# Kernel tuning notes

Measured on AMD Instinct MI355X. Metric: run time of the kernel, lower is better.

## Reference

```python
import jax, jax.numpy as jnp
import numpy as np

N_NODES = 50000


def sage_conv(x, edge_index, W_l, b_l, W_r):
    # PyG SAGEConv (mean aggr): out_i = lin_l(mean_{j->i} x_j) + lin_r(x_i)
    src, dst = edge_index[0], edge_index[1]
    msgs = x[src]                                        # [E, C] gather
    summed = jax.ops.segment_sum(msgs, dst, num_segments=N_NODES)  # [N, C]
    deg = jax.ops.segment_sum(jnp.ones((edge_index.shape[1],), x.dtype), dst,
                              num_segments=N_NODES)
    mean = summed / jnp.maximum(deg, 1.0)[:, None]
    return mean @ W_l + b_l + x @ W_r


def setup_inputs() -> dict:
    key = jax.random.key(0)
    ks = jax.random.split(key, 12)
    E, EL, C, X = 800000, 1000000, 128, 384
    return {
        "x": jax.random.normal(ks[0], (N_NODES, X), jnp.float32),
        "edge_index": jax.random.randint(ks[1], (2, E), 0, N_NODES),
        "edge_label_index": jax.random.randint(ks[2], (2, EL), 0, N_NODES),
        "W_lin": jax.random.normal(ks[3], (X, C), jnp.float32) * 0.05,
        "b_lin": jax.random.normal(ks[4], (C,), jnp.float32) * 0.05,
        "W1_l": jax.random.normal(ks[5], (C, C), jnp.float32) * 0.08,
        "b1": jax.random.normal(ks[6], (C,), jnp.float32) * 0.05,
        "W1_r": jax.random.normal(ks[7], (C, C), jnp.float32) * 0.08,
        "W2_l": jax.random.normal(ks[8], (C, C), jnp.float32) * 0.08,
        "b2": jax.random.normal(ks[9], (C,), jnp.float32) * 0.05,
        "W2_r": jax.random.normal(ks[10], (C, C), jnp.float32) * 0.08,
    }


def reference(x, edge_index, edge_label_index, W_lin, b_lin,
              W1_l, b1, W1_r, W2_l, b2, W2_r):
    h = x @ W_lin + b_lin                                # label_lin
    h = jax.nn.relu(sage_conv(h, edge_index, W1_l, b1, W1_r))
    h = sage_conv(h, edge_index, W2_l, b2, W2_r)
    # Classifier: dot product of head/tail node features per label edge
    head = h[edge_label_index[0]]
    tail = h[edge_label_index[1]]
    return (head * tail).sum(axis=-1)                    # [EL]
```

## Files before the change

### kernel.cpp

```cpp
#include <hip/hip_runtime.h>

#define NODES 50000
#define CH 128
#define ELLW 64

using frag_ab = __attribute__((ext_vector_type(8))) short;
using frag_cd = __attribute__((ext_vector_type(4))) float;

__device__ __forceinline__ float bf2f(ushort u) {
    union { unsigned u; float f; } v; v.u = ((unsigned)u) << 16; return v.f;
}
__device__ __forceinline__ ushort f2bf(float f) {
    union { float f; unsigned u; } v; v.f = f;
    unsigned r = v.u + 0x7fff + ((v.u >> 16) & 1);
    return (ushort)(r >> 16);
}

__global__ void prep_weights(const float* __restrict__ Wlin,
                             const float* __restrict__ W1l, const float* __restrict__ W1r,
                             const float* __restrict__ W2l, const float* __restrict__ W2r,
                             ushort* __restrict__ o0, ushort* __restrict__ o1,
                             ushort* __restrict__ o2, ushort* __restrict__ o3,
                             ushort* __restrict__ o4, int* __restrict__ deg) {
    int b = blockIdx.x;
    if (b >= 448) {
        int i = (b - 448) * 256 + threadIdx.y * 128 + threadIdx.x;
        if (i < NODES) deg[i] = 0;
        return;
    }
    const float* W; ushort* O; int K; int kb;
    if (b < 192) { W = Wlin; O = o0; K = 384; kb = b; }
    else {
        int j = (b - 192) >> 6; kb = (b - 192) & 63; K = 128;
        W = (j == 0) ? W1l : (j == 1) ? W1r : (j == 2) ? W2l : W2r;
        O = (j == 0) ? o1  : (j == 1) ? o2  : (j == 2) ? o3  : o4;
    }
    int k = kb * 2 + threadIdx.y;
    int n = threadIdx.x;
    if (k < K) O[(size_t)n * K + k] = f2bf(W[(size_t)k * 128 + n]);
}

__global__ void fill_ell(const int* __restrict__ ei, int E,
                         int* __restrict__ deg, int* __restrict__ ell) {
    int e = blockIdx.x * blockDim.x + threadIdx.x;
    if (e < E) {
        int d = ei[E + e];
        int pos = atomicAdd(&deg[d], 1);
        if (pos < ELLW) ell[(size_t)d * ELLW + pos] = ei[e];
    }
}

__device__ __forceinline__ void acc8(float* acc, uint4 v) {
    acc[0] += bf2f((ushort)(v.x & 0xffff)); acc[1] += bf2f((ushort)(v.x >> 16));
    acc[2] += bf2f((ushort)(v.y & 0xffff)); acc[3] += bf2f((ushort)(v.y >> 16));
    acc[4] += bf2f((ushort)(v.z & 0xffff)); acc[5] += bf2f((ushort)(v.z >> 16));
    acc[6] += bf2f((ushort)(v.w & 0xffff)); acc[7] += bf2f((ushort)(v.w >> 16));
}

__global__ __launch_bounds__(256) void aggregate_ell(
    const ushort* __restrict__ h, const int* __restrict__ ell,
    const int* __restrict__ deg, ushort* __restrict__ mean, int N) {
    int node = blockIdx.x * 4 + (threadIdx.x >> 6);
    if (node >= N) return;
    int lane = threadIdx.x & 63;
    int g = lane >> 4;
    int q = lane & 15;
    const int* row = ell + (size_t)node * ELLW;
    int d = deg[node];
    int dc = d < ELLW ? d : ELLW;

    float acc[8];
#pragma unroll
    for (int k = 0; k < 8; ++k) acc[k] = 0.f;

    int n = 0;
    for (; n + 16 <= dc; n += 16) {
        int i0 = row[n + g];
        int i1 = row[n + 4 + g];
        int i2 = row[n + 8 + g];
        int i3 = row[n + 12 + g];
        uint4 v0 = *(const uint4*)(h + (size_t)i0 * CH + q * 8);
        uint4 v1 = *(const uint4*)(h + (size_t)i1 * CH + q * 8);
        uint4 v2 = *(const uint4*)(h + (size_t)i2 * CH + q * 8);
        uint4 v3 = *(const uint4*)(h + (size_t)i3 * CH + q * 8);
        acc8(acc, v0); acc8(acc, v1); acc8(acc, v2); acc8(acc, v3);
    }
    for (; n + 8 <= dc; n += 8) {
        int i0 = row[n + g];
        int i1 = row[n + 4 + g];
        uint4 v0 = *(const uint4*)(h + (size_t)i0 * CH + q * 8);
        uint4 v1 = *(const uint4*)(h + (size_t)i1 * CH + q * 8);
        acc8(acc, v0); acc8(acc, v1);
    }
    for (; n < dc; n += 4) {
        int j = n + g;
        if (j < dc) {
            int i0 = row[j];
            uint4 v0 = *(const uint4*)(h + (size_t)i0 * CH + q * 8);
            acc8(acc, v0);
        }
    }
#pragma unroll
    for (int k = 0; k < 8; ++k) {
        acc[k] += __shfl_xor(acc[k], 16, 64);
        acc[k] += __shfl_xor(acc[k], 32, 64);
    }
    if (g == 0) {
        float inv = 1.f / fmaxf((float)d, 1.f);
        uint4 o;
        o.x = ((uint)f2bf(acc[1] * inv) << 16) | (uint)f2bf(acc[0] * inv);
        o.y = ((uint)f2bf(acc[3] * inv) << 16) | (uint)f2bf(acc[2] * inv);
        o.z = ((uint)f2bf(acc[5] * inv) << 16) | (uint)f2bf(acc[4] * inv);
        o.w = ((uint)f2bf(acc[7] * inv) << 16) | (uint)f2bf(acc[6] * inv);
        *(uint4*)(mean + (size_t)node * CH + q * 8) = o;
    }
}

__global__ __launch_bounds__(256) void gemm_lin(
    const float* __restrict__ A, const ushort* __restrict__ Wt,
    const float* __restrict__ bias, ushort* __restrict__ out, int N)
{
    __shared__ ushort As[128 * 32];
    __shared__ ushort Bs[128 * 32];
    const int tid = threadIdx.x;
    const int lane = tid & 63;
    const int wave = tid >> 6;
    const int wr = wave >> 1, wc = wave & 1;
    const int row0 = blockIdx.x * 128;
    const int l15 = lane & 15, quad = lane >> 4;

    frag_cd acc[4][4];
#pragma unroll
    for (int i = 0; i < 4; ++i)
#pragma unroll
        for (int j = 0; j < 4; ++j) acc[i][j] = (frag_cd){0.f, 0.f, 0.f, 0.f};

#pragma unroll 1
    for (int k0 = 0; k0 < 384; k0 += 32) {
        __syncthreads();
#pragma unroll
        for (int i = 0; i < 4; ++i) {
            int e = i * 256 + tid;
            int r = e >> 3, q = e & 7;
            int gr = row0 + r; if (gr > N - 1) gr = N - 1;
            float4 v = *(const float4*)(A + (size_t)gr * 384 + k0 + q * 4);
            ushort4 o; o.x = f2bf(v.x); o.y = f2bf(v.y); o.z = f2bf(v.z); o.w = f2bf(v.w);
            *(ushort4*)(As + r * 32 + q * 4) = o;
        }
#pragma unroll
        for (int i = 0; i < 2; ++i) {
            int e = i * 256 + tid;
            uint4 v = *(const uint4*)(Wt + (size_t)(e >> 2) * 384 + k0 + (e & 3) * 8);
            *(uint4*)(Bs + e * 8) = v;
        }
        __syncthreads();

        frag_ab a[4], b[4];
#pragma unroll
        for (int i = 0; i < 4; ++i)
            a[i] = *(const frag_ab*)(As + (wr * 64 + i * 16 + l15) * 32 + quad * 8);
#pragma unroll
        for (int j = 0; j < 4; ++j)
            b[j] = *(const frag_ab*)(Bs + (wc * 64 + j * 16 + l15) * 32 + quad * 8);
#pragma unroll
        for (int i = 0; i < 4; ++i)
#pragma unroll
            for (int j = 0; j < 4; ++j)
                acc[i][j] = __builtin_amdgcn_mfma_f32_16x16x32_bf16(a[i], b[j], acc[i][j], 0, 0, 0);
    }

#pragma unroll
    for (int i = 0; i < 4; ++i)
#pragma unroll
        for (int r = 0; r < 4; ++r) {
            int row = row0 + wr * 64 + i * 16 + quad * 4 + r;
            if (row < N)
#pragma unroll
                for (int j = 0; j < 4; ++j) {
                    int col = wc * 64 + j * 16 + l15;
                    out[(size_t)row * 128 + col] = f2bf(acc[i][j][r] + bias[col]);
                }
        }
}

template <bool RELU>
__global__ __launch_bounds__(256) void mfma_gemm(
    const ushort* __restrict__ A1, const ushort* __restrict__ Wt1,
    const ushort* __restrict__ A2, const ushort* __restrict__ Wt2,
    const float* __restrict__ bias, ushort* __restrict__ out, int N)
{
    __shared__ ushort As[128 * 32];
    __shared__ ushort Bs[128 * 32];
    const int tid = threadIdx.x;
    const int lane = tid & 63;
    const int wave = tid >> 6;
    const int wr = wave >> 1, wc = wave & 1;
    const int row0 = blockIdx.x * 128;
    const int l15 = lane & 15, quad = lane >> 4;

    frag_cd acc[4][4];
#pragma unroll
    for (int i = 0; i < 4; ++i)
#pragma unroll
        for (int j = 0; j < 4; ++j) acc[i][j] = (frag_cd){0.f, 0.f, 0.f, 0.f};

#pragma unroll 1
    for (int part = 0; part < 2; ++part) {
        const ushort* A  = part ? A2 : A1;
        const ushort* Wt = part ? Wt2 : Wt1;

#pragma unroll 1
        for (int k0 = 0; k0 < 128; k0 += 32) {
            __syncthreads();
#pragma unroll
            for (int i = 0; i < 2; ++i) {
                int e = i * 256 + tid;
                int r = e >> 2, kq = e & 3;
                int gr = row0 + r; if (gr > N - 1) gr = N - 1;
                uint4 v = *(const uint4*)(A + (size_t)gr * 128 + k0 + kq * 8);
                *(uint4*)(As + e * 8) = v;
            }
#pragma unroll
            for (int i = 0; i < 2; ++i) {
                int e = i * 256 + tid;
                uint4 v = *(const uint4*)(Wt + (size_t)(e >> 2) * 128 + k0 + (e & 3) * 8);
                *(uint4*)(Bs + e * 8) = v;
            }
            __syncthreads();

            frag_ab a[4], b[4];
#pragma unroll
            for (int i = 0; i < 4; ++i)
                a[i] = *(const frag_ab*)(As + (wr * 64 + i * 16 + l15) * 32 + quad * 8);
#pragma unroll
            for (int j = 0; j < 4; ++j)
                b[j] = *(const frag_ab*)(Bs + (wc * 64 + j * 16 + l15) * 32 + quad * 8);
#pragma unroll
            for (int i = 0; i < 4; ++i)
#pragma unroll
                for (int j = 0; j < 4; ++j)
                    acc[i][j] = __builtin_amdgcn_mfma_f32_16x16x32_bf16(a[i], b[j], acc[i][j], 0, 0, 0);
        }
    }

#pragma unroll
    for (int i = 0; i < 4; ++i)
#pragma unroll
        for (int r = 0; r < 4; ++r) {
            int row = row0 + wr * 64 + i * 16 + quad * 4 + r;
            if (row < N)
#pragma unroll
                for (int j = 0; j < 4; ++j) {
                    int col = wc * 64 + j * 16 + l15;
                    float v = acc[i][j][r] + bias[col];
                    if (RELU) v = fmaxf(v, 0.f);
                    out[(size_t)row * 128 + col] = f2bf(v);
                }
        }
}

__device__ __forceinline__ float dot8(uint4 va, uint4 vb) {
    float p = 0.f;
    p += bf2f((ushort)(va.x & 0xffff)) * bf2f((ushort)(vb.x & 0xffff));
    p += bf2f((ushort)(va.x >> 16))    * bf2f((ushort)(vb.x >> 16));
    p += bf2f((ushort)(va.y & 0xffff)) * bf2f((ushort)(vb.y & 0xffff));
    p += bf2f((ushort)(va.y >> 16))    * bf2f((ushort)(vb.y >> 16));
    p += bf2f((ushort)(va.z & 0xffff)) * bf2f((ushort)(vb.z & 0xffff));
    p += bf2f((ushort)(va.z >> 16))    * bf2f((ushort)(vb.z >> 16));
    p += bf2f((ushort)(va.w & 0xffff)) * bf2f((ushort)(vb.w & 0xffff));
    p += bf2f((ushort)(va.w >> 16))    * bf2f((ushort)(vb.w >> 16));
    return p;
}

__global__ __launch_bounds__(256) void classify_bf(
    const ushort* __restrict__ h2, const int* __restrict__ eli,
    int EL, float* __restrict__ out) {
    int gt = blockIdx.x * blockDim.x + threadIdx.x;
    int g0 = (gt >> 4) * 8;
    int lane = gt & 15;
    if (g0 >= EL) return;
    bool full = (g0 + 7 < EL);
    int ha[8], ta[8];
    if (full) {
        int4 h0 = *(const int4*)(eli + g0);
        int4 h1 = *(const int4*)(eli + g0 + 4);
        int4 t0 = *(const int4*)(eli + EL + g0);
        int4 t1 = *(const int4*)(eli + EL + g0 + 4);
        ha[0] = h0.x; ha[1] = h0.y; ha[2] = h0.z; ha[3] = h0.w;
        ha[4] = h1.x; ha[5] = h1.y; ha[6] = h1.z; ha[7] = h1.w;
        ta[0] = t0.x; ta[1] = t0.y; ta[2] = t0.z; ta[3] = t0.w;
        ta[4] = t1.x; ta[5] = t1.y; ta[6] = t1.z; ta[7] = t1.w;
    } else {
#pragma unroll
        for (int j = 0; j < 8; ++j) {
            int gj = (g0 + j < EL) ? g0 + j : EL - 1;
            ha[j] = eli[gj];
            ta[j] = eli[EL + gj];
        }
    }
    uint4 va[8], vb[8];
#pragma unroll
    for (int j = 0; j < 8; ++j) {
        va[j] = *((const uint4*)(h2 + (size_t)ha[j] * CH) + lane);
        vb[j] = *((const uint4*)(h2 + (size_t)ta[j] * CH) + lane);
    }
    float p[8];
#pragma unroll
    for (int j = 0; j < 8; ++j) p[j] = dot8(va[j], vb[j]);
#pragma unroll
    for (int s = 8; s >= 1; s >>= 1) {
#pragma unroll
        for (int j = 0; j < 8; ++j) p[j] += __shfl_down(p[j], s, 16);
    }
    if (lane == 0) {
        if (full) {
            *(float4*)(out + g0)     = make_float4(p[0], p[1], p[2], p[3]);
            *(float4*)(out + g0 + 4) = make_float4(p[4], p[5], p[6], p[7]);
        } else {
#pragma unroll
            for (int j = 0; j < 8; ++j)
                if (g0 + j < EL) out[g0 + j] = p[j];
        }
    }
}

extern "C" void kernel_launch(void* const* d_in, const int* in_sizes, int n_in,
                              void* d_out, int out_size, void* d_ws, size_t ws_size,
                              hipStream_t stream) {
    const float* x     = (const float*)d_in[0];
    const int*   ei    = (const int*)d_in[1];
    const int*   eli   = (const int*)d_in[2];
    const float* W_lin = (const float*)d_in[3];
    const float* b_lin = (const float*)d_in[4];
    const float* W1l   = (const float*)d_in[5];
    const float* b1    = (const float*)d_in[6];
    const float* W1r   = (const float*)d_in[7];
    const float* W2l   = (const float*)d_in[8];
    const float* b2    = (const float*)d_in[9];
    const float* W2r   = (const float*)d_in[10];
    float* out = (float*)d_out;

    const int E  = in_sizes[1] / 2;
    const int EL = in_sizes[2] / 2;
    const int N  = NODES;

    char* ws = (char*)d_ws;
    size_t off = 0;
    auto alloc = [&](size_t bytes) -> void* {
        void* p = ws + off;
        off += (bytes + 255) & ~(size_t)255;
        return p;
    };
    ushort* n0    = (ushort*)alloc((size_t)N * CH * sizeof(ushort));
    ushort* n1    = (ushort*)alloc((size_t)N * CH * sizeof(ushort));
    ushort* n2    = (ushort*)alloc((size_t)N * CH * sizeof(ushort));
    ushort* WtLin = (ushort*)alloc((size_t)CH * 384 * sizeof(ushort));
    ushort* Wt1l  = (ushort*)alloc((size_t)CH * CH * sizeof(ushort));
    ushort* Wt1r  = (ushort*)alloc((size_t)CH * CH * sizeof(ushort));
    ushort* Wt2l  = (ushort*)alloc((size_t)CH * CH * sizeof(ushort));
    ushort* Wt2r  = (ushort*)alloc((size_t)CH * CH * sizeof(ushort));
    int* deg = (int*)alloc((size_t)N * sizeof(int));
    int* ell = (int*)alloc((size_t)N * ELLW * sizeof(int));
    (void)ws_size; (void)n_in; (void)out_size;

    prep_weights<<<dim3(644), dim3(128, 2), 0, stream>>>(
        W_lin, W1l, W1r, W2l, W2r, WtLin, Wt1l, Wt1r, Wt2l, Wt2r, deg);

    fill_ell<<<dim3((E + 255) / 256), dim3(256), 0, stream>>>(ei, E, deg, ell);

    const int gblocks = (N + 127) / 128;
    const int ablocks = (N + 3) / 4;

    gemm_lin<<<dim3(gblocks), dim3(256), 0, stream>>>(x, WtLin, b_lin, n0, N);

    aggregate_ell<<<dim3(ablocks), dim3(256), 0, stream>>>(n0, ell, deg, n1, N);
    mfma_gemm<true><<<dim3(gblocks), dim3(256), 0, stream>>>(
        n1, Wt1l, n0, Wt1r, b1, n2, N);

    aggregate_ell<<<dim3(ablocks), dim3(256), 0, stream>>>(n2, ell, deg, n1, N);
    mfma_gemm<false><<<dim3(gblocks), dim3(256), 0, stream>>>(
        n1, Wt2l, n2, Wt2r, b2, n0, N);

    long long groups = ((long long)EL + 7) / 8;
    long long cls_threads = groups * 16;
    classify_bf<<<dim3((int)((cls_threads + 255) / 256)), dim3(256), 0, stream>>>(
        n0, eli, EL, out);
}
```

Measured before the change: 330.8 us.

## Co-schedule ELL build with input GEMM and aggregation with root-weight GEMM

Merges the ELL fill into the input linear GEMM launch as extra blocks, so edge scatter and GEMM run concurrently. Splits each SAGE layer's GEMM so the x@W_r half runs in the same launch as the neighbor aggregation. The remaining mean@W_l GEMM then adds the stored partial product, bias and ReLU. This hides the latency-bound gather and atomic work behind MFMA work and removes launches. The cost is an extra bf16 intermediate buffer that is written and read back, plus an extra rounding of the partial sum to bf16.

```diff
diff --git a/kernel.cpp b/kernel.cpp
--- a/kernel.cpp
+++ b/kernel.cpp
@@ -40,16 +40,6 @@
     if (k < K) O[(size_t)n * K + k] = f2bf(W[(size_t)k * 128 + n]);
 }
 
-__global__ void fill_ell(const int* __restrict__ ei, int E,
-                         int* __restrict__ deg, int* __restrict__ ell) {
-    int e = blockIdx.x * blockDim.x + threadIdx.x;
-    if (e < E) {
-        int d = ei[E + e];
-        int pos = atomicAdd(&deg[d], 1);
-        if (pos < ELLW) ell[(size_t)d * ELLW + pos] = ei[e];
-    }
-}
-
 __device__ __forceinline__ void acc8(float* acc, uint4 v) {
     acc[0] += bf2f((ushort)(v.x & 0xffff)); acc[1] += bf2f((ushort)(v.x >> 16));
     acc[2] += bf2f((ushort)(v.y & 0xffff)); acc[3] += bf2f((ushort)(v.y >> 16));
@@ -57,10 +47,10 @@
     acc[6] += bf2f((ushort)(v.w & 0xffff)); acc[7] += bf2f((ushort)(v.w >> 16));
 }
 
-__global__ __launch_bounds__(256) void aggregate_ell(
-    const ushort* __restrict__ h, const int* __restrict__ ell,
-    const int* __restrict__ deg, ushort* __restrict__ mean, int N) {
-    int node = blockIdx.x * 4 + (threadIdx.x >> 6);
+__device__ void agg4_dev(const ushort* __restrict__ h, const int* __restrict__ ell,
+                         const int* __restrict__ deg, ushort* __restrict__ mean,
+                         int N, int grp) {
+    int node = grp * 4 + (threadIdx.x >> 6);
     if (node >= N) return;
     int lane = threadIdx.x & 63;
     int g = lane >> 4;
@@ -116,9 +106,160 @@
     }
 }
 
-__global__ __launch_bounds__(256) void gemm_lin(
+__global__ __launch_bounds__(256) void lin_and_ell(
     const float* __restrict__ A, const ushort* __restrict__ Wt,
-    const float* __restrict__ bias, ushort* __restrict__ out, int N)
+    const float* __restrict__ bias, ushort* __restrict__ out, int N, int GB,
+    const int* __restrict__ ei, int E, int* __restrict__ deg, int* __restrict__ ell)
+{
+    __shared__ ushort As[128 * 32];
+    __shared__ ushort Bs[128 * 32];
+    if (blockIdx.x >= GB) {
+        int e = (blockIdx.x - GB) * 256 + threadIdx.x;
+        if (e < E) {
+            int d = ei[E + e];
+            int pos = atomicAdd(&deg[d], 1);
+            if (pos < ELLW) ell[(size_t)d * ELLW + pos] = ei[e];
+        }
+        return;
+    }
+    const int tid = threadIdx.x;
+    const int lane = tid & 63;
+    const int wave = tid >> 6;
+    const int wr = wave >> 1, wc = wave & 1;
+    const int row0 = blockIdx.x * 128;
+    const int l15 = lane & 15, quad = lane >> 4;
+
+    frag_cd acc[4][4];
+#pragma unroll
+    for (int i = 0; i < 4; ++i)
+#pragma unroll
+        for (int j = 0; j < 4; ++j) acc[i][j] = (frag_cd){0.f, 0.f, 0.f, 0.f};
+
+#pragma unroll 1
+    for (int k0 = 0; k0 < 384; k0 += 32) {
+        __syncthreads();
+#pragma unroll
+        for (int i = 0; i < 4; ++i) {
+            int e = i * 256 + tid;
+            int r = e >> 3, q = e & 7;
+            int gr = row0 + r; if (gr > N - 1) gr = N - 1;
+            float4 v = *(const float4*)(A + (size_t)gr * 384 + k0 + q * 4);
+            ushort4 o; o.x = f2bf(v.x); o.y = f2bf(v.y); o.z = f2bf(v.z); o.w = f2bf(v.w);
+            *(ushort4*)(As + r * 32 + q * 4) = o;
+        }
+#pragma unroll
+        for (int i = 0; i < 2; ++i) {
+            int e = i * 256 + tid;
+            uint4 v = *(const uint4*)(Wt + (size_t)(e >> 2) * 384 + k0 + (e & 3) * 8);
+            *(uint4*)(Bs + e * 8) = v;
+        }
+        __syncthreads();
+
+        frag_ab a[4], b[4];
+#pragma unroll
+        for (int i = 0; i < 4; ++i)
+            a[i] = *(const frag_ab*)(As + (wr * 64 + i * 16 + l15) * 32 + quad * 8);
+#pragma unroll
+        for (int j = 0; j < 4; ++j)
+            b[j] = *(const frag_ab*)(Bs + (wc * 64 + j * 16 + l15) * 32 + quad * 8);
+#pragma unroll
+        for (int i = 0; i < 4; ++i)
+#pragma unroll
+            for (int j = 0; j < 4; ++j)
+                acc[i][j] = __builtin_amdgcn_mfma_f32_16x16x32_bf16(a[i], b[j], acc[i][j], 0, 0, 0);
+    }
+
+#pragma unroll
+    for (int i = 0; i < 4; ++i)
+#pragma unroll
+        for (int r = 0; r < 4; ++r) {
+            int row = row0 + wr * 64 + i * 16 + quad * 4 + r;
+            if (row < N)
+#pragma unroll
+                for (int j = 0; j < 4; ++j) {
+                    int col = wc * 64 + j * 16 + l15;
+                    out[(size_t)row * 128 + col] = f2bf(acc[i][j][r] + bias[col]);
+                }
+        }
+}
+
+__global__ __launch_bounds__(256) void agg_gemmR(
+    const ushort* __restrict__ h, const ushort* __restrict__ Wtr,
+    ushort* __restrict__ t, int N, int GB,
+    const int* __restrict__ ell, const int* __restrict__ deg,
+    ushort* __restrict__ mean)
+{
+    __shared__ ushort As[128 * 32];
+    __shared__ ushort Bs[128 * 32];
+    if (blockIdx.x >= GB) {
+        agg4_dev(h, ell, deg, mean, N, blockIdx.x - GB);
+        return;
+    }
+    const int tid = threadIdx.x;
+    const int lane = tid & 63;
+    const int wave = tid >> 6;
+    const int wr = wave >> 1, wc = wave & 1;
+    const int row0 = blockIdx.x * 128;
+    const int l15 = lane & 15, quad = lane >> 4;
+
+    frag_cd acc[4][4];
+#pragma unroll
+    for (int i = 0; i < 4; ++i)
+#pragma unroll
+        for (int j = 0; j < 4; ++j) acc[i][j] = (frag_cd){0.f, 0.f, 0.f, 0.f};
+
+#pragma unroll 1
+    for (int k0 = 0; k0 < 128; k0 += 32) {
+        __syncthreads();
+#pragma unroll
+        for (int i = 0; i < 2; ++i) {
+            int e = i * 256 + tid;
+            int r = e >> 2, kq = e & 3;
+            int gr = row0 + r; if (gr > N - 1) gr = N - 1;
+            uint4 v = *(const uint4*)(h + (size_t)gr * 128 + k0 + kq * 8);
+            *(uint4*)(As + e * 8) = v;
+        }
+#pragma unroll
+        for (int i = 0; i < 2; ++i) {
+            int e = i * 256 + tid;
+            uint4 v = *(const uint4*)(Wtr + (size_t)(e >> 2) * 128 + k0 + (e & 3) * 8);
+            *(uint4*)(Bs + e * 8) = v;
+        }
+        __syncthreads();
+
+        frag_ab a[4], b[4];
+#pragma unroll
+        for (int i = 0; i < 4; ++i)
+            a[i] = *(const frag_ab*)(As + (wr * 64 + i * 16 + l15) * 32 + quad * 8);
+#pragma unroll
+        for (int j = 0; j < 4; ++j)
+            b[j] = *(const frag_ab*)(Bs + (wc * 64 + j * 16 + l15) * 32 + quad * 8);
+#pragma unroll
+        for (int i = 0; i < 4; ++i)
+#pragma unroll
+            for (int j = 0; j < 4; ++j)
+                acc[i][j] = __builtin_amdgcn_mfma_f32_16x16x32_bf16(a[i], b[j], acc[i][j], 0, 0, 0);
+    }
+
+#pragma unroll
+    for (int i = 0; i < 4; ++i)
+#pragma unroll
+        for (int r = 0; r < 4; ++r) {
+            int row = row0 + wr * 64 + i * 16 + quad * 4 + r;
+            if (row < N)
+#pragma unroll
+                for (int j = 0; j < 4; ++j) {
+                    int col = wc * 64 + j * 16 + l15;
+                    t[(size_t)row * 128 + col] = f2bf(acc[i][j][r]);
+                }
+        }
+}
+
+template <bool RELU>
+__global__ __launch_bounds__(256) void gemmL(
+    const ushort* __restrict__ mean, const ushort* __restrict__ Wtl,
+    const ushort* __restrict__ t, const float* __restrict__ bias,
+    ushort* __restrict__ out, int N)
 {
     __shared__ ushort As[128 * 32];
     __shared__ ushort Bs[128 * 32];
@@ -136,21 +277,20 @@
         for (int j = 0; j < 4; ++j) acc[i][j] = (frag_cd){0.f, 0.f, 0.f, 0.f};
 
 #pragma unroll 1
-    for (int k0 = 0; k0 < 384; k0 += 32) {
-        __syncthreads();
-#pragma unroll
-        for (int i = 0; i < 4; ++i) {
-            int e = i * 256 + tid;
-            int r = e >> 3, q = e & 7;
+    for (int k0 = 0; k0 < 128; k0 += 32) {
+        __syncthreads();
+#pragma unroll
+        for (int i = 0; i < 2; ++i) {
+            int e = i * 256 + tid;
+            int r = e >> 2, kq = e & 3;
             int gr = row0 + r; if (gr > N - 1) gr = N - 1;
-            float4 v = *(const float4*)(A + (size_t)gr * 384 + k0 + q * 4);
-            ushort4 o; o.x = f2bf(v.x); o.y = f2bf(v.y); o.z = f2bf(v.z); o.w = f2bf(v.w);
-            *(ushort4*)(As + r * 32 + q * 4) = o;
+            uint4 v = *(const uint4*)(mean + (size_t)gr * 128 + k0 + kq * 8);
+            *(uint4*)(As + e * 8) = v;
         }
 #pragma unroll
         for (int i = 0; i < 2; ++i) {
             int e = i * 256 + tid;
-            uint4 v = *(const uint4*)(Wt + (size_t)(e >> 2) * 384 + k0 + (e & 3) * 8);
+            uint4 v = *(const uint4*)(Wtl + (size_t)(e >> 2) * 128 + k0 + (e & 3) * 8);
             *(uint4*)(Bs + e * 8) = v;
         }
         __syncthreads();
@@ -178,81 +318,7 @@
 #pragma unroll
                 for (int j = 0; j < 4; ++j) {
                     int col = wc * 64 + j * 16 + l15;
-                    out[(size_t)row * 128 + col] = f2bf(acc[i][j][r] + bias[col]);
-                }
-        }
-}
-
-template <bool RELU>
-__global__ __launch_bounds__(256) void mfma_gemm(
-    const ushort* __restrict__ A1, const ushort* __restrict__ Wt1,
-    const ushort* __restrict__ A2, const ushort* __restrict__ Wt2,
-    const float* __restrict__ bias, ushort* __restrict__ out, int N)
-{
-    __shared__ ushort As[128 * 32];
-    __shared__ ushort Bs[128 * 32];
-    const int tid = threadIdx.x;
-    const int lane = tid & 63;
-    const int wave = tid >> 6;
-    const int wr = wave >> 1, wc = wave & 1;
-    const int row0 = blockIdx.x * 128;
-    const int l15 = lane & 15, quad = lane >> 4;
-
-    frag_cd acc[4][4];
-#pragma unroll
-    for (int i = 0; i < 4; ++i)
-#pragma unroll
-        for (int j = 0; j < 4; ++j) acc[i][j] = (frag_cd){0.f, 0.f, 0.f, 0.f};
-
-#pragma unroll 1
-    for (int part = 0; part < 2; ++part) {
-        const ushort* A  = part ? A2 : A1;
-        const ushort* Wt = part ? Wt2 : Wt1;
-
-#pragma unroll 1
-        for (int k0 = 0; k0 < 128; k0 += 32) {
-            __syncthreads();
-#pragma unroll
-            for (int i = 0; i < 2; ++i) {
-                int e = i * 256 + tid;
-                int r = e >> 2, kq = e & 3;
-                int gr = row0 + r; if (gr > N - 1) gr = N - 1;
-                uint4 v = *(const uint4*)(A + (size_t)gr * 128 + k0 + kq * 8);
-                *(uint4*)(As + e * 8) = v;
-            }
-#pragma unroll
-            for (int i = 0; i < 2; ++i) {
-                int e = i * 256 + tid;
-                uint4 v = *(const uint4*)(Wt + (size_t)(e >> 2) * 128 + k0 + (e & 3) * 8);
-                *(uint4*)(Bs + e * 8) = v;
-            }
-            __syncthreads();
-
-            frag_ab a[4], b[4];
-#pragma unroll
-            for (int i = 0; i < 4; ++i)
-                a[i] = *(const frag_ab*)(As + (wr * 64 + i * 16 + l15) * 32 + quad * 8);
-#pragma unroll
-            for (int j = 0; j < 4; ++j)
-                b[j] = *(const frag_ab*)(Bs + (wc * 64 + j * 16 + l15) * 32 + quad * 8);
-#pragma unroll
-            for (int i = 0; i < 4; ++i)
-#pragma unroll
-                for (int j = 0; j < 4; ++j)
-                    acc[i][j] = __builtin_amdgcn_mfma_f32_16x16x32_bf16(a[i], b[j], acc[i][j], 0, 0, 0);
-        }
-    }
-
-#pragma unroll
-    for (int i = 0; i < 4; ++i)
-#pragma unroll
-        for (int r = 0; r < 4; ++r) {
-            int row = row0 + wr * 64 + i * 16 + quad * 4 + r;
-            if (row < N)
-#pragma unroll
-                for (int j = 0; j < 4; ++j) {
-                    int col = wc * 64 + j * 16 + l15;
-                    float v = acc[i][j][r] + bias[col];
+                    float v = acc[i][j][r] + bf2f(t[(size_t)row * 128 + col]) + bias[col];
                     if (RELU) v = fmaxf(v, 0.f);
                     out[(size_t)row * 128 + col] = f2bf(v);
                 }
@@ -354,6 +420,7 @@
     ushort* n0    = (ushort*)alloc((size_t)N * CH * sizeof(ushort));
     ushort* n1    = (ushort*)alloc((size_t)N * CH * sizeof(ushort));
     ushort* n2    = (ushort*)alloc((size_t)N * CH * sizeof(ushort));
+    ushort* n3    = (ushort*)alloc((size_t)N * CH * sizeof(ushort));
     ushort* WtLin = (ushort*)alloc((size_t)CH * 384 * sizeof(ushort));
     ushort* Wt1l  = (ushort*)alloc((size_t)CH * CH * sizeof(ushort));
     ushort* Wt1r  = (ushort*)alloc((size_t)CH * CH * sizeof(ushort));
@@ -363,23 +430,23 @@
     int* ell = (int*)alloc((size_t)N * ELLW * sizeof(int));
     (void)ws_size; (void)n_in; (void)out_size;
 
+    const int GB = (N + 127) / 128;
+    const int EB = (E + 255) / 256;
+    const int AB = (N + 3) / 4;
+
     prep_weights<<<dim3(644), dim3(128, 2), 0, stream>>>(
         W_lin, W1l, W1r, W2l, W2r, WtLin, Wt1l, Wt1r, Wt2l, Wt2r, deg);
 
-    fill_ell<<<dim3((E + 255) / 256), dim3(256), 0, stream>>>(ei, E, deg, ell);
-
-    const int gblocks = (N + 127) / 128;
-    const int ablocks = (N + 3) / 4;
-
-    gemm_lin<<<dim3(gblocks), dim3(256), 0, stream>>>(x, WtLin, b_lin, n0, N);
-
-    aggregate_ell<<<dim3(ablocks), dim3(256), 0, stream>>>(n0, ell, deg, n1, N);
-    mfma_gemm<true><<<dim3(gblocks), dim3(256), 0, stream>>>(
-        n1, Wt1l, n0, Wt1r, b1, n2, N);
-
-    aggregate_ell<<<dim3(ablocks), dim3(256), 0, stream>>>(n2, ell, deg, n1, N);
-    mfma_gemm<false><<<dim3(gblocks), dim3(256), 0, stream>>>(
-        n1, Wt2l, n2, Wt2r, b2, n0, N);
+    lin_and_ell<<<dim3(GB + EB), dim3(256), 0, stream>>>(
+        x, WtLin, b_lin, n0, N, GB, ei, E, deg, ell);
+
+    agg_gemmR<<<dim3(GB + AB), dim3(256), 0, stream>>>(
+        n0, Wt1r, n3, N, GB, ell, deg, n1);
+    gemmL<true><<<dim3(GB), dim3(256), 0, stream>>>(n1, Wt1l, n3, b1, n2, N);
+
+    agg_gemmR<<<dim3(GB + AB), dim3(256), 0, stream>>>(
+        n2, Wt2r, n3, N, GB, ell, deg, n1);
+    gemmL<false><<<dim3(GB), dim3(256), 0, stream>>>(n1, Wt2l, n3, b2, n0, N);
 
     long long groups = ((long long)EL + 7) / 8;
     long long cls_threads = groups * 16;
```

New measurement: 355.4 us. +7.4%, slower.
